# Kernel optimization log

Measured on AMD Instinct MI355X. Metric: run time of the kernel, lower is better.

## Reference

```python
import jax, jax.numpy as jnp
import numpy as np

N_TOKENS = 32768
D_MODEL = 1024
TOT_EXPERT = 16
TOP_K = 2


def setup_inputs() -> dict:
    key = jax.random.key(0)
    k1, k2 = jax.random.split(key)
    inp = jax.random.normal(k1, (N_TOKENS, D_MODEL), dtype=jnp.float32)
    # nn.Linear(d_model, tot_expert, bias=False) weight: [tot_expert, d_model]
    W = jax.random.normal(k2, (TOT_EXPERT, D_MODEL), dtype=jnp.float32) * 0.02
    return {"inp": inp, "W": W}


def reference(inp, W):
    # gate logits: [N, E]
    logits = jnp.einsum('nd,ed->ne', inp, W)
    # top-k over experts (sorted order differs from torch sorted=False, but the
    # selected set and the downstream math are identical)
    top_k_logits, top_k_indices = jax.lax.top_k(logits, TOP_K)  # [N, K]
    # scatter top-k logits into a -inf buffer, then softmax over experts
    rows = jnp.arange(inp.shape[0])[:, None]
    router = jnp.full_like(logits, -jnp.inf).at[rows, top_k_indices].set(top_k_logits)
    router_probs = jax.nn.softmax(router, axis=-1)  # [N, E]
    # load-balance loss: f_i (no-grad expert selection freq) dot P_i (mean prob)
    f_i = jnp.zeros((TOT_EXPERT,), jnp.float32).at[top_k_indices.reshape(-1)].add(1.0) / inp.shape[0]
    P_i = jnp.mean(router_probs.astype(jnp.float32), axis=0)
    loss = jnp.sum(jax.lax.stop_gradient(f_i) * P_i) * TOT_EXPERT
    # gather the softmaxed scores of the selected experts
    top_k_scores = jnp.take_along_axis(router_probs, top_k_indices, axis=-1)  # [N, K]
    return top_k_indices, top_k_scores, loss
```

## Files before the change

kernel.cpp:

```cpp
#include <hip/hip_runtime.h>
#include <math.h>

#define N_TOKENS 32768
#define D_MODEL  1024
#define N_EXPERT 16
#define TPB      256
#define NBLK     1024
#define TOKS     32
#define BATCH    16

typedef float f32x4 __attribute__((ext_vector_type(4)));
typedef float f32x2 __attribute__((ext_vector_type(2)));

template<int CTRL>
static __device__ __forceinline__ float dpp_xor(float v) {
    return __int_as_float(__builtin_amdgcn_update_dpp(
        0, __float_as_int(v), CTRL, 0xF, 0xF, true));
}

static __device__ __forceinline__ float dot4pk(f32x4 x, f32x4 w) {
    f32x2 xl = __builtin_shufflevector(x, x, 0, 1);
    f32x2 xh = __builtin_shufflevector(x, x, 2, 3);
    f32x2 wl = __builtin_shufflevector(w, w, 0, 1);
    f32x2 wh = __builtin_shufflevector(w, w, 2, 3);
    f32x2 m, r;
    asm("v_pk_mul_f32 %0, %1, %2" : "=v"(m) : "v"(xl), "v"(wl));
    asm("v_pk_fma_f32 %0, %1, %2, %3" : "=v"(r) : "v"(xh), "v"(wh), "v"(m));
    return r.x + r.y;
}


__global__ __launch_bounds__(256, 4)
void gate_kernel(const float* __restrict__ inp,
                 const float* __restrict__ W,
                 float* __restrict__ out,
                 float* __restrict__ ws)
{
    const int tid  = threadIdx.x;
    const int wave = tid >> 6;
    const int lane = tid & 63;
    const int p    = lane & 15;
    const int d0   = wave * 256 + lane * 4;
    const int base = blockIdx.x * TOKS;

    f32x4 wreg[N_EXPERT];
    #pragma unroll
    for (int j = 0; j < N_EXPERT; ++j)
        wreg[j] = *reinterpret_cast<const f32x4*>(W + (j ^ p) * D_MODEL + d0);

    __shared__ float lds_part[2][BATCH][4][N_EXPERT];
    __shared__ float lds_red[4][2][N_EXPERT];

    float cnt_acc = 0.f;
    float ps_acc  = 0.f;

    const float* xptr = inp + (size_t)base * D_MODEL + d0;

#define LOADX(xr, t) xr = *reinterpret_cast<const f32x4*>(xptr + (size_t)(t) * D_MODEL);

#define DOTOK(xv, slot, BUF) do { \
    float a0 =dot4pk(xv,wreg[0]),  a1 =dot4pk(xv,wreg[1]);  \
    float a2 =dot4pk(xv,wreg[2]),  a3 =dot4pk(xv,wreg[3]);  \
    float a4 =dot4pk(xv,wreg[4]),  a5 =dot4pk(xv,wreg[5]);  \
    float a6 =dot4pk(xv,wreg[6]),  a7 =dot4pk(xv,wreg[7]);  \
    float a8 =dot4pk(xv,wreg[8]),  a9 =dot4pk(xv,wreg[9]);  \
    float a10=dot4pk(xv,wreg[10]), a11=dot4pk(xv,wreg[11]); \
    float a12=dot4pk(xv,wreg[12]), a13=dot4pk(xv,wreg[13]); \
    float a14=dot4pk(xv,wreg[14]), a15=dot4pk(xv,wreg[15]); \
    float b0 = a0 + dpp_xor<0x128>(a8);  \
    float b1 = a1 + dpp_xor<0x128>(a9);  \
    float b2 = a2 + dpp_xor<0x128>(a10); \
    float b3 = a3 + dpp_xor<0x128>(a11); \
    float b4 = a4 + dpp_xor<0x128>(a12); \
    float b5 = a5 + dpp_xor<0x128>(a13); \
    float b6 = a6 + dpp_xor<0x128>(a14); \
    float b7 = a7 + dpp_xor<0x128>(a15); \
    float c0 = b0 + __shfl_xor(b4, 4); \
    float c1 = b1 + __shfl_xor(b5, 4); \
    float c2 = b2 + __shfl_xor(b6, 4); \
    float c3 = b3 + __shfl_xor(b7, 4); \
    float d0_ = c0 + dpp_xor<0x4E>(c2); \
    float d1_ = c1 + dpp_xor<0x4E>(c3); \
    float s0  = d0_ + dpp_xor<0xB1>(d1_); \
    s0 += __shfl_xor(s0, 16); \
    s0 += __shfl_xor(s0, 32); \
    if (lane < N_EXPERT) BUF[slot][wave][lane] = s0; \
} while (0)

#define PHASEB(BUF, TOKBASE) do { \
    const int tgrp = tid >> 4; \
    const int el   = tid & 15; \
    float v1 = BUF[tgrp][0][el] + BUF[tgrp][1][el] \
             + BUF[tgrp][2][el] + BUF[tgrp][3][el]; \
    int   i1 = el; \
    float v2 = -INFINITY; \
    int   i2 = 0; \
    _Pragma("unroll") \
    for (int m = 1; m <= 8; m <<= 1) { \
        float o1 = __shfl_xor(v1, m); \
        int  oi1 = __shfl_xor(i1, m); \
        float o2 = __shfl_xor(v2, m); \
        int  oi2 = __shfl_xor(i2, m); \
        bool afirst = (v1 > o1) || (v1 == o1 && i1 < oi1); \
        float c1v = afirst ? v1 : o1;   int c1i = afirst ? i1 : oi1; \
        float bv  = afirst ? o1 : v1;   int bi  = afirst ? oi1 : i1; \
        float sv  = afirst ? v2 : o2;   int si  = afirst ? i2 : oi2; \
        bool sgt  = (bv > sv) || (bv == sv && bi < si); \
        v1 = c1v; i1 = c1i; \
        v2 = sgt ? bv : sv;  i2 = sgt ? bi : si; \
    } \
    float tt = expf(v2 - v1); \
    float p1 = 1.f / (1.f + tt); \
    float p2 = tt * p1; \
    const int tok = (TOKBASE) + tgrp; \
    if (el == 0) { \
        *reinterpret_cast<float2*>(out + 2 * tok) = \
            make_float2((float)i1, (float)i2); \
        *reinterpret_cast<float2*>(out + 2 * N_TOKENS + 2 * tok) = \
            make_float2(p1, p2); \
    } \
    cnt_acc += (el == i1 ? 1.f : 0.f) + (el == i2 ? 1.f : 0.f); \
    ps_acc  += (el == i1 ? p1  : 0.f) + (el == i2 ? p2  : 0.f); \
} while (0)

    f32x4 x0, x1, x2, x3;

    LOADX(x0, 0) LOADX(x1, 1) LOADX(x2, 2) LOADX(x3, 3)
    for (int g = 0; g < 3; ++g) {
        const int t = g * 4;
        DOTOK(x0, t + 0, lds_part[0]); LOADX(x0, t + 4)
        DOTOK(x1, t + 1, lds_part[0]); LOADX(x1, t + 5)
        DOTOK(x2, t + 2, lds_part[0]); LOADX(x2, t + 6)
        DOTOK(x3, t + 3, lds_part[0]); LOADX(x3, t + 7)
    }
    DOTOK(x0, 12, lds_part[0]); LOADX(x0, 16)
    DOTOK(x1, 13, lds_part[0]); LOADX(x1, 17)
    DOTOK(x2, 14, lds_part[0]); LOADX(x2, 18)
    DOTOK(x3, 15, lds_part[0]); LOADX(x3, 19)

    __syncthreads();
    PHASEB(lds_part[0], base);

    for (int g = 0; g < 3; ++g) {
        const int t = 16 + g * 4;
        DOTOK(x0, (t + 0) & 15, lds_part[1]); LOADX(x0, t + 4)
        DOTOK(x1, (t + 1) & 15, lds_part[1]); LOADX(x1, t + 5)
        DOTOK(x2, (t + 2) & 15, lds_part[1]); LOADX(x2, t + 6)
        DOTOK(x3, (t + 3) & 15, lds_part[1]); LOADX(x3, t + 7)
    }
    DOTOK(x0, 12, lds_part[1]);
    DOTOK(x1, 13, lds_part[1]);
    DOTOK(x2, 14, lds_part[1]);
    DOTOK(x3, 15, lds_part[1]);

    __syncthreads();
    PHASEB(lds_part[1], base + 16);

    cnt_acc += __shfl_xor(cnt_acc, 16); cnt_acc += __shfl_xor(cnt_acc, 32);
    ps_acc  += __shfl_xor(ps_acc, 16);  ps_acc  += __shfl_xor(ps_acc, 32);
    __syncthreads();
    if (lane < N_EXPERT) {
        lds_red[wave][0][lane] = cnt_acc;
        lds_red[wave][1][lane] = ps_acc;
    }
    __syncthreads();
    if (tid < 32) {
        const int el = tid & 15;
        const int which = tid >> 4;
        float v = lds_red[0][which][el] + lds_red[1][which][el]
                + lds_red[2][which][el] + lds_red[3][which][el];
        ws[blockIdx.x * 32 + tid] = v;
    }
#undef LOADX
#undef DOTOK
#undef PHASEB
}

__global__ void loss_kernel(const float* __restrict__ ws, float* __restrict__ out)
{
    __shared__ float partial[8][32];
    __shared__ float col[32];
    const int tid = threadIdx.x;
    const int c   = tid & 31;
    const int ch  = tid >> 5;
    float s0 = 0.f, s1 = 0.f, s2 = 0.f, s3 = 0.f;
    for (int b = 0; b < NBLK / 8; b += 4) {
        s0 += ws[(size_t)(ch * (NBLK / 8) + b + 0) * 32 + c];
        s1 += ws[(size_t)(ch * (NBLK / 8) + b + 1) * 32 + c];
        s2 += ws[(size_t)(ch * (NBLK / 8) + b + 2) * 32 + c];
        s3 += ws[(size_t)(ch * (NBLK / 8) + b + 3) * 32 + c];
    }
    partial[ch][c] = (s0 + s1) + (s2 + s3);
    __syncthreads();
    if (tid < 32) {
        float t = 0.f;
        #pragma unroll
        for (int k = 0; k < 8; ++k) t += partial[k][tid];
        col[tid] = t;
    }
    __syncthreads();
    if (tid == 0) {
        float sum = 0.f;
        #pragma unroll
        for (int e = 0; e < N_EXPERT; ++e)
            sum += col[e] * col[16 + e];
        out[4 * N_TOKENS] = sum * (float)N_EXPERT
                          / ((float)N_TOKENS * (float)N_TOKENS);
    }
}

extern "C" void kernel_launch(void* const* d_in, const int* in_sizes, int n_in,
                              void* d_out, int out_size, void* d_ws, size_t ws_size,
                              hipStream_t stream)
{
    const float* inp = (const float*)d_in[0];
    const float* W   = (const float*)d_in[1];
    float* out = (float*)d_out;
    float* ws  = (float*)d_ws;

    gate_kernel<<<NBLK, TPB, 0, stream>>>(inp, W, out, ws);
    loss_kernel<<<1, 256, 0, stream>>>(ws, out);
}
```

Measured before the change: 37.71 us.

## Deepen input prefetch to eight tokens and widen loss reduction kernel

The gate kernel now keeps eight token rows of input in flight per thread instead of four, fully unrolling the dot-product schedule to hide more global-load latency. A redundant barrier before the per-wave reduction store is dropped. The loss kernel is relaunched with 1024 threads so each thread sums 32 partials instead of 128, shortening its serial reduction. The extra live vector registers (on top of 16 weight vectors) risk pressure against the 4-blocks-per-SM launch bound.

After: 48.18 us. 27.8% more time.

```diff
diff --git a/kernel.cpp b/kernel.cpp
--- a/kernel.cpp
+++ b/kernel.cpp
@@ -123,42 +123,52 @@
     ps_acc  += (el == i1 ? p1  : 0.f) + (el == i2 ? p2  : 0.f); \
 } while (0)
 
-    f32x4 x0, x1, x2, x3;
-
+    f32x4 x0, x1, x2, x3, x4, x5, x6, x7;
     LOADX(x0, 0) LOADX(x1, 1) LOADX(x2, 2) LOADX(x3, 3)
-    for (int g = 0; g < 3; ++g) {
-        const int t = g * 4;
-        DOTOK(x0, t + 0, lds_part[0]); LOADX(x0, t + 4)
-        DOTOK(x1, t + 1, lds_part[0]); LOADX(x1, t + 5)
-        DOTOK(x2, t + 2, lds_part[0]); LOADX(x2, t + 6)
-        DOTOK(x3, t + 3, lds_part[0]); LOADX(x3, t + 7)
-    }
-    DOTOK(x0, 12, lds_part[0]); LOADX(x0, 16)
-    DOTOK(x1, 13, lds_part[0]); LOADX(x1, 17)
-    DOTOK(x2, 14, lds_part[0]); LOADX(x2, 18)
-    DOTOK(x3, 15, lds_part[0]); LOADX(x3, 19)
+    LOADX(x4, 4) LOADX(x5, 5) LOADX(x6, 6) LOADX(x7, 7)
+
+    DOTOK(x0,  0, lds_part[0]); LOADX(x0,  8)
+    DOTOK(x1,  1, lds_part[0]); LOADX(x1,  9)
+    DOTOK(x2,  2, lds_part[0]); LOADX(x2, 10)
+    DOTOK(x3,  3, lds_part[0]); LOADX(x3, 11)
+    DOTOK(x4,  4, lds_part[0]); LOADX(x4, 12)
+    DOTOK(x5,  5, lds_part[0]); LOADX(x5, 13)
+    DOTOK(x6,  6, lds_part[0]); LOADX(x6, 14)
+    DOTOK(x7,  7, lds_part[0]); LOADX(x7, 15)
+    DOTOK(x0,  8, lds_part[0]); LOADX(x0, 16)
+    DOTOK(x1,  9, lds_part[0]); LOADX(x1, 17)
+    DOTOK(x2, 10, lds_part[0]); LOADX(x2, 18)
+    DOTOK(x3, 11, lds_part[0]); LOADX(x3, 19)
+    DOTOK(x4, 12, lds_part[0]); LOADX(x4, 20)
+    DOTOK(x5, 13, lds_part[0]); LOADX(x5, 21)
+    DOTOK(x6, 14, lds_part[0]); LOADX(x6, 22)
+    DOTOK(x7, 15, lds_part[0]); LOADX(x7, 23)
 
     __syncthreads();
     PHASEB(lds_part[0], base);
 
-    for (int g = 0; g < 3; ++g) {
-        const int t = 16 + g * 4;
-        DOTOK(x0, (t + 0) & 15, lds_part[1]); LOADX(x0, t + 4)
-        DOTOK(x1, (t + 1) & 15, lds_part[1]); LOADX(x1, t + 5)
-        DOTOK(x2, (t + 2) & 15, lds_part[1]); LOADX(x2, t + 6)
-        DOTOK(x3, (t + 3) & 15, lds_part[1]); LOADX(x3, t + 7)
-    }
-    DOTOK(x0, 12, lds_part[1]);
-    DOTOK(x1, 13, lds_part[1]);
-    DOTOK(x2, 14, lds_part[1]);
-    DOTOK(x3, 15, lds_part[1]);
+    DOTOK(x0,  0, lds_part[1]); LOADX(x0, 24)
+    DOTOK(x1,  1, lds_part[1]); LOADX(x1, 25)
+    DOTOK(x2,  2, lds_part[1]); LOADX(x2, 26)
+    DOTOK(x3,  3, lds_part[1]); LOADX(x3, 27)
+    DOTOK(x4,  4, lds_part[1]); LOADX(x4, 28)
+    DOTOK(x5,  5, lds_part[1]); LOADX(x5, 29)
+    DOTOK(x6,  6, lds_part[1]); LOADX(x6, 30)
+    DOTOK(x7,  7, lds_part[1]); LOADX(x7, 31)
+    DOTOK(x0,  8, lds_part[1]);
+    DOTOK(x1,  9, lds_part[1]);
+    DOTOK(x2, 10, lds_part[1]);
+    DOTOK(x3, 11, lds_part[1]);
+    DOTOK(x4, 12, lds_part[1]);
+    DOTOK(x5, 13, lds_part[1]);
+    DOTOK(x6, 14, lds_part[1]);
+    DOTOK(x7, 15, lds_part[1]);
 
     __syncthreads();
     PHASEB(lds_part[1], base + 16);
 
     cnt_acc += __shfl_xor(cnt_acc, 16); cnt_acc += __shfl_xor(cnt_acc, 32);
     ps_acc  += __shfl_xor(ps_acc, 16);  ps_acc  += __shfl_xor(ps_acc, 32);
-    __syncthreads();
     if (lane < N_EXPERT) {
         lds_red[wave][0][lane] = cnt_acc;
         lds_red[wave][1][lane] = ps_acc;
@@ -176,26 +186,28 @@
 #undef PHASEB
 }
 
-__global__ void loss_kernel(const float* __restrict__ ws, float* __restrict__ out)
+__global__ __launch_bounds__(1024)
+void loss_kernel(const float* __restrict__ ws, float* __restrict__ out)
 {
-    __shared__ float partial[8][32];
+    __shared__ float red[32][33];
     __shared__ float col[32];
     const int tid = threadIdx.x;
     const int c   = tid & 31;
-    const int ch  = tid >> 5;
+    const int r   = tid >> 5;
     float s0 = 0.f, s1 = 0.f, s2 = 0.f, s3 = 0.f;
-    for (int b = 0; b < NBLK / 8; b += 4) {
-        s0 += ws[(size_t)(ch * (NBLK / 8) + b + 0) * 32 + c];
-        s1 += ws[(size_t)(ch * (NBLK / 8) + b + 1) * 32 + c];
-        s2 += ws[(size_t)(ch * (NBLK / 8) + b + 2) * 32 + c];
-        s3 += ws[(size_t)(ch * (NBLK / 8) + b + 3) * 32 + c];
-    }
-    partial[ch][c] = (s0 + s1) + (s2 + s3);
+    #pragma unroll
+    for (int k = 0; k < 32; k += 4) {
+        s0 += ws[(size_t)(r + (k + 0) * 32) * 32 + c];
+        s1 += ws[(size_t)(r + (k + 1) * 32) * 32 + c];
+        s2 += ws[(size_t)(r + (k + 2) * 32) * 32 + c];
+        s3 += ws[(size_t)(r + (k + 3) * 32) * 32 + c];
+    }
+    red[r][c] = (s0 + s1) + (s2 + s3);
     __syncthreads();
     if (tid < 32) {
         float t = 0.f;
         #pragma unroll
-        for (int k = 0; k < 8; ++k) t += partial[k][tid];
+        for (int k = 0; k < 32; ++k) t += red[k][tid];
         col[tid] = t;
     }
     __syncthreads();
@@ -219,5 +231,5 @@
     float* ws  = (float*)d_ws;
 
     gate_kernel<<<NBLK, TPB, 0, stream>>>(inp, W, out, ws);
-    loss_kernel<<<1, 256, 0, stream>>>(ws, out);
-}
+    loss_kernel<<<1, 1024, 0, stream>>>(ws, out);
+}
```
